# Kernel optimization log

Hardware: AMD Instinct MI355X
Metric: run time of the kernel (lower is better)

Reference implementation:

```python
import jax, jax.numpy as jnp
import numpy as np

GRID_SIZE = 8
POS_MARGIN = 1.0
NEG_MARGIN = 0.2
LOSS_LAMBDA = 1.0
NEG_PER_POS = 374.359


def gaussian_kernel1d(ks, sigma):
    x = jnp.arange(ks, dtype=jnp.float32) - (ks - 1) / 2.0
    k = jnp.exp(-(x * x) / (2.0 * sigma * sigma))
    return k / k.sum()


def gaussian_filter(x, ks, sigma):
    # x: [B,1,H,W]; normalized 2D gaussian = outer product of 1D gaussians -> separable
    k = gaussian_kernel1d(ks, sigma).astype(x.dtype)
    pad = ks // 2
    x = jax.lax.conv_general_dilated(x, k.reshape(1, 1, ks, 1), (1, 1), [(pad, pad), (0, 0)])
    x = jax.lax.conv_general_dilated(x, k.reshape(1, 1, 1, ks), (1, 1), [(0, 0), (pad, pad)])
    return x


def space_to_depth(x, bs):
    n, c, h, w = x.shape
    x = x.reshape(n, c, h // bs, bs, w // bs, bs)
    x = x.transpose(0, 3, 5, 1, 2, 4)
    return x.reshape(n, c * bs * bs, h // bs, w // bs)


def sample_descriptors(desc, kp, grid_size):
    # desc: N x C x Hr x Wr; kp: K x 4 = (batch_idx, score, y, x) in full-res pixels
    n, c, hr, wr = desc.shape
    b = kp[:, 0].astype(jnp.int32)
    y = kp[:, 2] / grid_size
    x = kp[:, 3] / grid_size
    x0 = jnp.clip(jnp.floor(x), 0, wr - 1)
    y0 = jnp.clip(jnp.floor(y), 0, hr - 1)
    x1 = jnp.clip(x0 + 1, 0, wr - 1)
    y1 = jnp.clip(y0 + 1, 0, hr - 1)
    wx = (x - x0)[:, None]
    wy = (y - y0)[:, None]
    x0i, x1i = x0.astype(jnp.int32), x1.astype(jnp.int32)
    y0i, y1i = y0.astype(jnp.int32), y1.astype(jnp.int32)
    d00 = desc[b, :, y0i, x0i]  # K x C
    d01 = desc[b, :, y0i, x1i]
    d10 = desc[b, :, y1i, x0i]
    d11 = desc[b, :, y1i, x1i]
    return d00 * (1 - wx) * (1 - wy) + d01 * wx * (1 - wy) + d10 * (1 - wx) * wy + d11 * wx * wy


def setup_inputs() -> dict:
    key = jax.random.key(0)
    k1, k2, k3, k4, k5, k6 = jax.random.split(key, 6)
    N, C, Hr, Wr, K = 8, 128, 32, 32, 1024
    H, W = Hr * GRID_SIZE, Wr * GRID_SIZE
    desc1 = jax.random.normal(k1, (N, C, Hr, Wr), jnp.float32) / np.sqrt(C)
    desc2 = jax.random.normal(k2, (N, C, Hr, Wr), jnp.float32) / np.sqrt(C)
    # keypoints: (batch_idx, score, y, x) with y,x in full-res pixels
    b = jax.random.randint(k3, (K,), 0, N).astype(jnp.float32)
    y = jax.random.uniform(k4, (K,), jnp.float32, 0.0, H - 1.0)
    x = jax.random.uniform(k5, (K,), jnp.float32, 0.0, W - 1.0)
    kp1 = jnp.stack([b, jnp.zeros((K,), jnp.float32), y, x], axis=1)
    # near-identity homographies so s is non-trivial
    homo21 = jnp.eye(3, dtype=jnp.float32)[None] + 0.001 * jax.random.normal(k6, (N, 3, 3), jnp.float32)
    vis_mask1 = jnp.ones((N, 1, H, W), jnp.float32)
    return {"kp1": kp1, "desc1": desc1, "desc2": desc2, "homo21": homo21, "vis_mask1": vis_mask1}


def reference(kp1, desc1, desc2, homo21, vis_mask1):
    n, c, hr, wr = desc2.shape
    K = kp1.shape[0]
    # keypoint (x, y) in full-res pixels
    kp_grid = kp1[:, jnp.array([3, 2])].astype(jnp.float32)  # K x 2
    # warped grid of reduced-cell centers (full-res coords)
    ys, xs = jnp.meshgrid(jnp.arange(hr, dtype=jnp.float32), jnp.arange(wr, dtype=jnp.float32), indexing='ij')
    grid = jnp.stack([xs, ys], axis=-1) * GRID_SIZE + GRID_SIZE // 2  # Hr x Wr x 2
    pts = jnp.concatenate([grid, jnp.ones((hr, wr, 1), jnp.float32)], axis=-1)
    wp = jnp.einsum('nij,hwj->nhwi', homo21, pts)
    w_grid = wp[..., :2] / wp[..., 2:3]  # N x Hr x Wr x 2

    vis = space_to_depth(vis_mask1, GRID_SIZE).prod(axis=1).reshape(n, 1, hr, wr)

    diff = kp_grid[None, :, None, None, :] - w_grid[:, None]  # N x K x Hr x Wr x 2
    grid_dist = jnp.sqrt(jnp.sum(diff * diff, axis=-1))
    s = jnp.where(grid_dist <= GRID_SIZE - 0.5, 1.0, 0.0).astype(desc2.dtype)  # N x K x Hr x Wr

    ns_in = s.reshape(-1, 1, hr, wr)
    ns = (gaussian_filter(ns_in, 31, 7.0)
          + gaussian_filter(ns_in, 11, 4.0)
          + gaussian_filter(ns_in, 5, 2.0)).reshape(n, K, hr, wr) - 3.0 * s

    s = s * vis
    ns = ns * vis

    kp1_desc = sample_descriptors(desc1, kp1, GRID_SIZE)  # K x C
    dot_desc = jnp.einsum('kc,nchw->nkhw', kp1_desc, desc2)  # N x K x Hr x Wr

    pos_dist = jnp.maximum(POS_MARGIN - dot_desc, 0.0)
    neg_dist = jnp.maximum(dot_desc - NEG_MARGIN, 0.0)
    pos_lambda = NEG_PER_POS * 0.3
    loss = (pos_lambda * s * pos_dist + ns * neg_dist).sum() / (K * NEG_PER_POS) * LOSS_LAMBDA
    return loss, kp1_desc
```

## Files before the change

### kernel.cpp

```cpp
#include <hip/hip_runtime.h>
#include <math.h>

using short8 = __attribute__((ext_vector_type(8))) short;
using f32x4v = __attribute__((ext_vector_type(4))) float;

__device__ __forceinline__ short f2bf(float f) {
  unsigned u = __builtin_bit_cast(unsigned, f);
  unsigned r = (u + 0x7fffu + ((u >> 16) & 1u)) >> 16;
  return (short)r;
}

__global__ __launch_bounds__(256) void prep_kernel(
    const float* __restrict__ kp1, const float* __restrict__ desc1,
    const float* __restrict__ desc2, const float* __restrict__ homo,
    const float* __restrict__ vism, float* __restrict__ okpd,
    float* __restrict__ visg, int* __restrict__ cntw, int* __restrict__ cellw,
    short* __restrict__ kpdb, short* __restrict__ d2t,
    float* __restrict__ stampg,
    float inv31sq, float inv11sq, float inv5sq) {
  __shared__ short tile[128][33];
  __shared__ int cnt[32];
  __shared__ int cells[32][8];
  __shared__ float kx[32], ky[32];

  const int bid = blockIdx.x;
  const int t = threadIdx.x;

  if (bid < 256) {
    int n = bid & 7, q = bid >> 3;
#pragma unroll
    for (int pass = 0; pass < 4; ++pass) {
      int c = pass * 32 + (t >> 3);
      int px4 = (t & 7) * 4;
      float4 f = *(const float4*)(desc2 + ((size_t)n * 128 + c) * 1024 +
                                  q * 32 + px4);
      tile[c][px4] = f2bf(f.x);
      tile[c][px4 + 1] = f2bf(f.y);
      tile[c][px4 + 2] = f2bf(f.z);
      tile[c][px4 + 3] = f2bf(f.w);
    }
    __syncthreads();
#pragma unroll
    for (int pass = 0; pass < 2; ++pass) {
      int px = pass * 16 + (t >> 4);
      int ch = (t & 15) * 8;
      short8 o;
#pragma unroll
      for (int j = 0; j < 8; ++j) o[j] = tile[ch + j][px];
      *(short8*)(d2t + ((size_t)n * 1024 + q * 32 + px) * 128 + ch) = o;
    }
  } else if (bid < 320) {
    int idx = bid - 256;
    int n = idx & 7, seg = idx >> 3;
    int cell = seg * 128 + (t >> 1);
    int ph = cell >> 5, pw = cell & 31;
    const float* mrow =
        vism + ((size_t)n * 256 + ph * 8 + (t & 1) * 4) * 256 + pw * 8;
    float v = 1.f;
#pragma unroll
    for (int dy = 0; dy < 4; ++dy) {
      const float4* p = (const float4*)(mrow + dy * 256);
      float4 a = p[0], b = p[1];
      v *= a.x * a.y * a.z * a.w;
      v *= b.x * b.y * b.z * b.w;
    }
    float pv = __shfl_xor(v, 1, 64);
    v *= pv;
    if ((t & 1) == 0) visg[n * 1024 + cell] = v;
  } else if (bid < 832) {
    int k = (bid - 320) * 2 + (t >> 7);
    int c = t & 127;
    float b = kp1[k * 4 + 0];
    float y = kp1[k * 4 + 2] * 0.125f;
    float x = kp1[k * 4 + 3] * 0.125f;
    float x0 = fminf(fmaxf(floorf(x), 0.f), 31.f);
    float y0 = fminf(fmaxf(floorf(y), 0.f), 31.f);
    float x1 = fminf(x0 + 1.f, 31.f);
    float y1 = fminf(y0 + 1.f, 31.f);
    float wx = x - x0;
    float wy = y - y0;
    const float* dp = desc1 + ((size_t)(int)b * 128 + c) * 1024;
    const float* r0 = dp + (int)y0 * 32;
    const float* r1 = dp + (int)y1 * 32;
    float d00 = r0[(int)x0];
    float d01 = r0[(int)x1];
    float d10 = r1[(int)x0];
    float d11 = r1[(int)x1];
    float r = d00 * (1.f - wx) * (1.f - wy) + d01 * wx * (1.f - wy)
            + d10 * (1.f - wx) * wy + d11 * wx * wy;
    okpd[k * 128 + c] = r;
    kpdb[k * 128 + c] = f2bf(r);
  } else if (bid < 1088) {
    int idx = bid - 832;
    int n = idx & 7;
    int kp0 = (idx >> 3) * 32;
    if (t < 32) {
      cnt[t] = 0;
      kx[t] = kp1[(kp0 + t) * 4 + 3];
      ky[t] = kp1[(kp0 + t) * 4 + 2];
    }
    __syncthreads();
    const float h00 = homo[n * 9 + 0], h01 = homo[n * 9 + 1], h02 = homo[n * 9 + 2];
    const float h10 = homo[n * 9 + 3], h11 = homo[n * 9 + 4], h12 = homo[n * 9 + 5];
    const float h20 = homo[n * 9 + 6], h21 = homo[n * 9 + 7], h22 = homo[n * 9 + 8];
#pragma unroll
    for (int i = 0; i < 4; ++i) {
      int cell = t + 256 * i;
      int ph = cell >> 5, pw = cell & 31;
      float gx = (float)(pw * 8 + 4);
      float gy = (float)(ph * 8 + 4);
      float w0 = h00 * gx + h01 * gy + h02;
      float w1 = h10 * gx + h11 * gy + h12;
      float w2 = h20 * gx + h21 * gy + h22;
      float wx_ = w0 / w2, wy_ = w1 / w2;
#pragma unroll
      for (int kt = 0; kt < 32; ++kt) {
        float dx = kx[kt] - wx_;
        float dy = ky[kt] - wy_;
        if (dx * dx + dy * dy <= 56.25f) {
          int pos = atomicAdd(&cnt[kt], 1);
          if (pos < 8) cells[kt][pos] = cell;
        }
      }
    }
    __syncthreads();
    if (t < 32) cntw[n * 1024 + kp0 + t] = min(cnt[t], 8);
    cellw[(size_t)(n * 1024 + kp0) * 8 + t] = cells[t >> 3][t & 7];
  } else {
    for (int i = t; i < 63 * 64; i += 256) {
      int yy = i >> 6, xx = i & 63;
      int dy = yy - 16, dx = xx - 16;
      float v = 0.f;
      if ((unsigned)dy < 31u && (unsigned)dx < 31u) {
        float ay = (float)(dy - 15), ax = (float)(dx - 15);
        float r2 = ay * ay + ax * ax;
        v = expf(r2 * (-1.f / 98.f)) * inv31sq;
        if (dy >= 10 && dy <= 20 && dx >= 10 && dx <= 20)
          v += expf(r2 * (-1.f / 32.f)) * inv11sq;
        if (dy >= 13 && dy <= 17 && dx >= 13 && dx <= 17)
          v += expf(r2 * (-1.f / 8.f)) * inv5sq;
      }
      stampg[i] = v;
    }
  }
}

__global__ __launch_bounds__(256, 3) void main_kernel(
    const float* __restrict__ kp1, const float* __restrict__ homo,
    const float* __restrict__ visg, const int* __restrict__ cntw,
    const int* __restrict__ cellw, const short* __restrict__ kpdb,
    const short* __restrict__ d2t, const float* __restrict__ stampg,
    float* __restrict__ part) {
  __shared__ short sB[128 * 128];
  __shared__ float s_T[35 * 64];
  __shared__ float s_wx[128], s_wy[128], s_vis[128];
  __shared__ float s_kpx[128], s_kpy[128];
  __shared__ int s_cnt[128];
  __shared__ int s_cells[1024];
  __shared__ float s_red[4];

  const int t = threadIdx.x;
  const int bid = blockIdx.x;
  const int n = bid & 7;
  const int rem = bid >> 3;
  const int k0 = (rem & 7) * 128;
  const int p0 = (rem >> 3) * 128;
  const int ph0 = p0 >> 5;

  {
    const short* gB = d2t + ((size_t)n * 1024 + p0) * 128;
#pragma unroll
    for (int i = 0; i < 8; ++i) {
      int idx = t + 256 * i;
      int px = idx >> 4, u = idx & 15;
      short8 v = *(const short8*)(gB + idx * 8);
      *(short8*)((char*)sB + px * 256 + ((u ^ (px & 7)) << 4)) = v;
    }
  }
  for (int i = t; i < 35 * 64; i += 256) s_T[i] = stampg[ph0 * 64 + i];
  if (t < 128) {
    int pxg = p0 + t;
    int ph = pxg >> 5, pw = pxg & 31;
    float gx = (float)(pw * 8 + 4);
    float gy = (float)(ph * 8 + 4);
    float w0 = homo[n * 9 + 0] * gx + homo[n * 9 + 1] * gy + homo[n * 9 + 2];
    float w1 = homo[n * 9 + 3] * gx + homo[n * 9 + 4] * gy + homo[n * 9 + 5];
    float w2 = homo[n * 9 + 6] * gx + homo[n * 9 + 7] * gy + homo[n * 9 + 8];
    s_wx[t] = w0 / w2;
    s_wy[t] = w1 / w2;
    s_vis[t] = visg[n * 1024 + pxg];
    s_kpx[t] = kp1[(k0 + t) * 4 + 3];
    s_kpy[t] = kp1[(k0 + t) * 4 + 2];
    s_cnt[t] = cntw[n * 1024 + k0 + t];
  }
#pragma unroll
  for (int i = 0; i < 4; ++i)
    s_cells[t + 256 * i] = cellw[(size_t)(n * 1024 + k0) * 8 + t + 256 * i];
  __syncthreads();

  const int w = t >> 6, l = t & 63;
  const int lr = l & 15, lh = l >> 4;
  const float POSL = 112.30770111083984f;
  float lp = 0.f;

#pragma unroll
  for (int pass = 0; pass < 2; ++pass) {
    const int kb = pass * 64;

    const short* Abase =
        kpdb + (size_t)(k0 + kb + (w << 4) + lr) * 128 + lh * 8;
    short8 af[4];
#pragma unroll
    for (int ks = 0; ks < 4; ++ks) af[ks] = *(const short8*)(Abase + ks * 32);

    f32x4v acc[8];
#pragma unroll
    for (int nt = 0; nt < 8; ++nt) {
      acc[nt] = (f32x4v){0.f, 0.f, 0.f, 0.f};
      int pxl = nt * 16 + lr;
      const char* brow = (const char*)sB + pxl * 256;
      int sw = (pxl & 7);
#pragma unroll
      for (int ks = 0; ks < 4; ++ks) {
        short8 bf = *(const short8*)(brow + (((lh + 4 * ks) ^ sw) << 4));
        acc[nt] = __builtin_amdgcn_mfma_f32_16x16x32_bf16(af[ks], bf, acc[nt],
                                                          0, 0, 0);
      }
    }

    float blur[8][4];
#pragma unroll
    for (int nt = 0; nt < 8; ++nt)
#pragma unroll
      for (int r = 0; r < 4; ++r) blur[nt][r] = 0.f;
#pragma unroll
    for (int r = 0; r < 4; ++r) {
      int kp = kb + (w << 4) + (lh << 2) + r;
      int cn = s_cnt[kp];
      for (int j = 0; j < cn; ++j) {
        int cell = s_cells[kp * 8 + j];
        int row0 = 31 - (cell >> 5);
        int xbase = lr - (cell & 31) + 31;
#pragma unroll
        for (int nt = 0; nt < 8; ++nt)
          blur[nt][r] += s_T[(row0 + (nt >> 1)) * 64 + xbase + (nt & 1) * 16];
      }
    }

#pragma unroll
    for (int nt = 0; nt < 8; ++nt) {
      int pxl = nt * 16 + lr;
      float wx_ = s_wx[pxl], wy_ = s_wy[pxl], vv = s_vis[pxl];
#pragma unroll
      for (int r = 0; r < 4; ++r) {
        int kp = kb + (w << 4) + (lh << 2) + r;
        float dx = s_kpx[kp] - wx_;
        float dy = s_kpy[kp] - wy_;
        float sval = (dx * dx + dy * dy <= 56.25f) ? 1.f : 0.f;
        float dot = acc[nt][r];
        float pos = fmaxf(1.f - dot, 0.f);
        float neg = fmaxf(dot - 0.2f, 0.f);
        lp = fmaf(POSL * sval * vv, pos, lp);
        lp = fmaf((blur[nt][r] - 3.f * sval) * vv, neg, lp);
      }
    }
  }

#pragma unroll
  for (int off = 32; off > 0; off >>= 1) lp += __shfl_down(lp, off, 64);
  if ((t & 63) == 0) s_red[t >> 6] = lp;
  __syncthreads();
  if (t == 0)
    part[bid] = (s_red[0] + s_red[1]) + (s_red[2] + s_red[3]);
}

__global__ void reduce_kernel(const float* __restrict__ part,
                              float* __restrict__ out) {
  __shared__ float s_red[4];
  int t = threadIdx.x;
  float v = part[t] + part[t + 256];
#pragma unroll
  for (int off = 32; off > 0; off >>= 1) v += __shfl_down(v, off, 64);
  if ((t & 63) == 0) s_red[t >> 6] = v;
  __syncthreads();
  if (t == 0)
    out[0] = ((s_red[0] + s_red[1]) + (s_red[2] + s_red[3])) *
             (float)(1.0 / (1024.0 * 374.359));
}

extern "C" void kernel_launch(void* const* d_in, const int* in_sizes, int n_in,
                              void* d_out, int out_size, void* d_ws, size_t ws_size,
                              hipStream_t stream) {
  (void)in_sizes; (void)n_in; (void)out_size; (void)ws_size;
  const float* kp1   = (const float*)d_in[0];
  const float* desc1 = (const float*)d_in[1];
  const float* desc2 = (const float*)d_in[2];
  const float* homo  = (const float*)d_in[3];
  const float* vism  = (const float*)d_in[4];
  float* out = (float*)d_out;

  float* visg   = (float*)d_ws;
  int*   cntw   = (int*)(visg + 8192);
  int*   cellw  = cntw + 8192;
  short* kpdb   = (short*)(cellw + 65536);
  short* d2t    = kpdb + 131072;
  float* part   = (float*)(d2t + 1048576);
  float* stampg = part + 1024;

  auto ksum = [](int ks, double sigma) {
    double sum = 0.0;
    for (int i = 0; i < ks; ++i) {
      double x = i - (ks - 1) / 2.0;
      sum += exp(-(x * x) / (2.0 * sigma * sigma));
    }
    return sum;
  };
  double s31 = ksum(31, 7.0), s11 = ksum(11, 4.0), s5 = ksum(5, 2.0);
  float inv31sq = (float)(1.0 / (s31 * s31));
  float inv11sq = (float)(1.0 / (s11 * s11));
  float inv5sq  = (float)(1.0 / (s5 * s5));

  prep_kernel<<<dim3(1089), dim3(256), 0, stream>>>(
      kp1, desc1, desc2, homo, vism, out + 1, visg, cntw, cellw, kpdb, d2t,
      stampg, inv31sq, inv11sq, inv5sq);
  main_kernel<<<dim3(512), dim3(256), 0, stream>>>(
      kp1, homo, visg, cntw, cellw, kpdb, d2t, stampg, part);
  reduce_kernel<<<dim3(1), dim3(256), 0, stream>>>(part, out);
}
```

Measured before the change: 40.26 us.

## Double main kernel block size to 8 waves, one keypoint row-slice per wave

The main kernel now launches 512 threads per block instead of 256. Each of the eight waves handles 16 keypoints in a single pass rather than two passes of 64 keypoints over four waves. The blur accumulation is restructured per keypoint row to shrink the live register set, and launch bounds are raised to allow more waves per CU. This aims to increase latency hiding and parallelism in the MFMA and blur stages, at the cost of tighter register limits and more threads sharing the same LDS tile.

```diff
diff --git a/kernel.cpp b/kernel.cpp
--- a/kernel.cpp
+++ b/kernel.cpp
@@ -145,7 +145,7 @@
   }
 }
 
-__global__ __launch_bounds__(256, 3) void main_kernel(
+__global__ __launch_bounds__(512, 6) void main_kernel(
     const float* __restrict__ kp1, const float* __restrict__ homo,
     const float* __restrict__ visg, const int* __restrict__ cntw,
     const int* __restrict__ cellw, const short* __restrict__ kpdb,
@@ -157,7 +157,7 @@
   __shared__ float s_kpx[128], s_kpy[128];
   __shared__ int s_cnt[128];
   __shared__ int s_cells[1024];
-  __shared__ float s_red[4];
+  __shared__ float s_red[8];
 
   const int t = threadIdx.x;
   const int bid = blockIdx.x;
@@ -170,14 +170,14 @@
   {
     const short* gB = d2t + ((size_t)n * 1024 + p0) * 128;
 #pragma unroll
-    for (int i = 0; i < 8; ++i) {
-      int idx = t + 256 * i;
+    for (int i = 0; i < 4; ++i) {
+      int idx = t + 512 * i;
       int px = idx >> 4, u = idx & 15;
       short8 v = *(const short8*)(gB + idx * 8);
       *(short8*)((char*)sB + px * 256 + ((u ^ (px & 7)) << 4)) = v;
     }
   }
-  for (int i = t; i < 35 * 64; i += 256) s_T[i] = stampg[ph0 * 64 + i];
+  for (int i = t; i < 35 * 64; i += 512) s_T[i] = stampg[ph0 * 64 + i];
   if (t < 128) {
     int pxg = p0 + t;
     int ph = pxg >> 5, pw = pxg & 31;
@@ -189,89 +189,80 @@
     s_wx[t] = w0 / w2;
     s_wy[t] = w1 / w2;
     s_vis[t] = visg[n * 1024 + pxg];
-    s_kpx[t] = kp1[(k0 + t) * 4 + 3];
-    s_kpy[t] = kp1[(k0 + t) * 4 + 2];
-    s_cnt[t] = cntw[n * 1024 + k0 + t];
-  }
-#pragma unroll
-  for (int i = 0; i < 4; ++i)
-    s_cells[t + 256 * i] = cellw[(size_t)(n * 1024 + k0) * 8 + t + 256 * i];
+  } else if (t < 256) {
+    int kk = t - 128;
+    s_kpx[kk] = kp1[(k0 + kk) * 4 + 3];
+    s_kpy[kk] = kp1[(k0 + kk) * 4 + 2];
+    s_cnt[kk] = cntw[n * 1024 + k0 + kk];
+  }
+#pragma unroll
+  for (int i = 0; i < 2; ++i)
+    s_cells[t + 512 * i] = cellw[(size_t)(n * 1024 + k0) * 8 + t + 512 * i];
   __syncthreads();
 
   const int w = t >> 6, l = t & 63;
   const int lr = l & 15, lh = l >> 4;
+  const short* Abase = kpdb + (size_t)(k0 + (w << 4) + lr) * 128 + lh * 8;
+  short8 af[4];
+#pragma unroll
+  for (int ks = 0; ks < 4; ++ks) af[ks] = *(const short8*)(Abase + ks * 32);
+
+  f32x4v acc[8];
+#pragma unroll
+  for (int nt = 0; nt < 8; ++nt) {
+    acc[nt] = (f32x4v){0.f, 0.f, 0.f, 0.f};
+    int pxl = nt * 16 + lr;
+    const char* brow = (const char*)sB + pxl * 256;
+    int sw = (pxl & 7);
+#pragma unroll
+    for (int ks = 0; ks < 4; ++ks) {
+      short8 bf = *(const short8*)(brow + (((lh + 4 * ks) ^ sw) << 4));
+      acc[nt] =
+          __builtin_amdgcn_mfma_f32_16x16x32_bf16(af[ks], bf, acc[nt], 0, 0, 0);
+    }
+  }
+
   const float POSL = 112.30770111083984f;
   float lp = 0.f;
-
-#pragma unroll
-  for (int pass = 0; pass < 2; ++pass) {
-    const int kb = pass * 64;
-
-    const short* Abase =
-        kpdb + (size_t)(k0 + kb + (w << 4) + lr) * 128 + lh * 8;
-    short8 af[4];
-#pragma unroll
-    for (int ks = 0; ks < 4; ++ks) af[ks] = *(const short8*)(Abase + ks * 32);
-
-    f32x4v acc[8];
-#pragma unroll
-    for (int nt = 0; nt < 8; ++nt) {
-      acc[nt] = (f32x4v){0.f, 0.f, 0.f, 0.f};
-      int pxl = nt * 16 + lr;
-      const char* brow = (const char*)sB + pxl * 256;
-      int sw = (pxl & 7);
-#pragma unroll
-      for (int ks = 0; ks < 4; ++ks) {
-        short8 bf = *(const short8*)(brow + (((lh + 4 * ks) ^ sw) << 4));
-        acc[nt] = __builtin_amdgcn_mfma_f32_16x16x32_bf16(af[ks], bf, acc[nt],
-                                                          0, 0, 0);
-      }
-    }
-
-    float blur[8][4];
-#pragma unroll
-    for (int nt = 0; nt < 8; ++nt)
-#pragma unroll
-      for (int r = 0; r < 4; ++r) blur[nt][r] = 0.f;
-#pragma unroll
-    for (int r = 0; r < 4; ++r) {
-      int kp = kb + (w << 4) + (lh << 2) + r;
-      int cn = s_cnt[kp];
-      for (int j = 0; j < cn; ++j) {
-        int cell = s_cells[kp * 8 + j];
-        int row0 = 31 - (cell >> 5);
-        int xbase = lr - (cell & 31) + 31;
-#pragma unroll
-        for (int nt = 0; nt < 8; ++nt)
-          blur[nt][r] += s_T[(row0 + (nt >> 1)) * 64 + xbase + (nt & 1) * 16];
-      }
-    }
-
+#pragma unroll
+  for (int r = 0; r < 4; ++r) {
+    int kp = (w << 4) + (lh << 2) + r;
+    float bl[8];
+#pragma unroll
+    for (int nt = 0; nt < 8; ++nt) bl[nt] = 0.f;
+    int cn = s_cnt[kp];
+    for (int j = 0; j < cn; ++j) {
+      int cell = s_cells[kp * 8 + j];
+      int row0 = 31 - (cell >> 5);
+      int xbase = lr - (cell & 31) + 31;
+#pragma unroll
+      for (int nt = 0; nt < 8; ++nt)
+        bl[nt] += s_T[(row0 + (nt >> 1)) * 64 + xbase + (nt & 1) * 16];
+    }
+    float kpx = s_kpx[kp], kpy = s_kpy[kp];
 #pragma unroll
     for (int nt = 0; nt < 8; ++nt) {
       int pxl = nt * 16 + lr;
       float wx_ = s_wx[pxl], wy_ = s_wy[pxl], vv = s_vis[pxl];
-#pragma unroll
-      for (int r = 0; r < 4; ++r) {
-        int kp = kb + (w << 4) + (lh << 2) + r;
-        float dx = s_kpx[kp] - wx_;
-        float dy = s_kpy[kp] - wy_;
-        float sval = (dx * dx + dy * dy <= 56.25f) ? 1.f : 0.f;
-        float dot = acc[nt][r];
-        float pos = fmaxf(1.f - dot, 0.f);
-        float neg = fmaxf(dot - 0.2f, 0.f);
-        lp = fmaf(POSL * sval * vv, pos, lp);
-        lp = fmaf((blur[nt][r] - 3.f * sval) * vv, neg, lp);
-      }
-    }
-  }
-
+      float dx = kpx - wx_;
+      float dy = kpy - wy_;
+      float sval = (dx * dx + dy * dy <= 56.25f) ? 1.f : 0.f;
+      float dot = acc[nt][r];
+      float pos = fmaxf(1.f - dot, 0.f);
+      float neg = fmaxf(dot - 0.2f, 0.f);
+      lp = fmaf(POSL * sval * vv, pos, lp);
+      lp = fmaf((bl[nt] - 3.f * sval) * vv, neg, lp);
+    }
+  }
 #pragma unroll
   for (int off = 32; off > 0; off >>= 1) lp += __shfl_down(lp, off, 64);
   if ((t & 63) == 0) s_red[t >> 6] = lp;
   __syncthreads();
-  if (t == 0)
-    part[bid] = (s_red[0] + s_red[1]) + (s_red[2] + s_red[3]);
+  if (t == 0) {
+    float tot = ((s_red[0] + s_red[1]) + (s_red[2] + s_red[3])) +
+                ((s_red[4] + s_red[5]) + (s_red[6] + s_red[7]));
+    part[bid] = tot;
+  }
 }
 
 __global__ void reduce_kernel(const float* __restrict__ part,
@@ -323,7 +314,7 @@
   prep_kernel<<<dim3(1089), dim3(256), 0, stream>>>(
       kp1, desc1, desc2, homo, vism, out + 1, visg, cntw, cellw, kpdb, d2t,
       stampg, inv31sq, inv11sq, inv5sq);
-  main_kernel<<<dim3(512), dim3(256), 0, stream>>>(
+  main_kernel<<<dim3(512), dim3(512), 0, stream>>>(
       kp1, homo, visg, cntw, cellw, kpdb, d2t, stampg, part);
   reduce_kernel<<<dim3(1), dim3(256), 0, stream>>>(part, out);
 }
```

New measurement: 58.47 us. 1.45x slower.
